# Optimization experiments

Hardware: AMD Instinct MI355X
Metric: run time of the kernel (lower is better)

The kernel has to match this reference:

```python
import jax, jax.numpy as jnp
import numpy as np

B, S, E, HD = 32, 1024, 768, 64


def _rope_tables(seq_len, dim):
    # theta = 10000 ** (-2*arange(0,dim,2)/dim); freqs = pos * theta
    theta = jnp.power(10000.0, -2.0 * jnp.arange(0, dim, 2, dtype=jnp.float32) / dim)
    pos = jnp.arange(seq_len, dtype=jnp.float32)[:, None]          # [S,1]
    freqs = pos * theta[None, :]                                    # [S,dim//2]
    cos = jnp.repeat(jnp.cos(freqs), 2, axis=-1)                    # [S,dim]
    sin = jnp.repeat(jnp.sin(freqs), 2, axis=-1)                    # [S,dim]
    return cos, sin


def _apply_rope(x, cos, sin):
    # rotate-half interleaved: new[...,0::2] = -x[...,1::2]; new[...,1::2] = x[...,0::2]
    b, s, d = x.shape
    x2 = x.reshape(b, s, d // 2, 2)
    rot = jnp.stack([-x2[..., 1], x2[..., 0]], axis=-1).reshape(b, s, d)
    return x * cos[None] + rot * sin[None]


def setup_inputs() -> dict:
    key = jax.random.key(0)
    k0, k1, k2, k3 = jax.random.split(key, 4)
    x = jax.random.normal(k0, (B, S, E), dtype=jnp.float32)
    Wq = jax.random.normal(k1, (HD, E), dtype=jnp.float32) * 0.02
    Wk = jax.random.normal(k2, (HD, E), dtype=jnp.float32) * 0.02
    Wv = jax.random.normal(k3, (HD, E), dtype=jnp.float32) * 0.02
    return {"x": x, "Wq": Wq, "Wk": Wk, "Wv": Wv}


def reference(x, Wq, Wk, Wv):
    b, s, e = x.shape
    q = jnp.einsum('bse,he->bsh', x, Wq)
    k = jnp.einsum('bse,he->bsh', x, Wk)
    v = jnp.einsum('bse,he->bsh', x, Wv)
    cos, sin = _rope_tables(s, q.shape[-1])
    rq = _apply_rope(q, cos, sin)
    rk = _apply_rope(k, cos, sin)
    scale = e ** (-0.5)  # NOTE: original scales by emb_dim, not head_size
    scores = jnp.einsum('bqh,bkh->bqk', rq, rk) * scale
    causal = jnp.tril(jnp.ones((s, s), dtype=bool))
    scores = jnp.where(causal[None], scores, -jnp.inf)
    attn = jax.nn.softmax(scores, axis=-1)
    return jnp.einsum('bqk,bkh->bqh', attn, v)
```

## Files before the change

kernel.cpp:

```cpp
#include <hip/hip_runtime.h>
#include <hip/hip_bf16.h>

#define B_  32
#define S_  1024
#define E_  768
#define HD_ 64
#define M_  (B_*S_)
#define WREP 8
#define WPSZ 147456

typedef __attribute__((ext_vector_type(8))) short short8;
typedef __attribute__((ext_vector_type(4))) float float4v;

__device__ __forceinline__ unsigned short f2bf(float x) {
    union { float f; unsigned u; } c; c.f = x;
    unsigned r = (c.u + 0x7FFFu + ((c.u >> 16) & 1u)) >> 16;
    return (unsigned short)r;
}

__device__ __forceinline__ void gld_lds16(const void* g, void* l) {
    __builtin_amdgcn_global_load_lds(
        (const __attribute__((address_space(1))) unsigned int*)g,
        (__attribute__((address_space(3))) unsigned int*)l,
        16, 0, 0);
}

__global__ __launch_bounds__(256) void setup_kernel(
    const unsigned int* __restrict__ xw,
    const void* __restrict__ Wq_, const void* __restrict__ Wk_,
    const void* __restrict__ Wv_,
    unsigned int* __restrict__ flag,
    float* __restrict__ cs_t, float* __restrict__ sn_t,
    unsigned short* __restrict__ wp)
{
    const int bx = blockIdx.x;
    if (bx < 128) {
        int idx = bx * 256 + threadIdx.x;
        int pos = idx >> 5;
        int ii  = idx & 31;
        float theta = exp2f(-(float)ii * 0.8304820237218406f);
        float fr = (float)pos * theta;
        float sn, cs;
        sincosf(fr, &sn, &cs);
        cs_t[idx] = cs;
        sn_t[idx] = sn;
        return;
    }
    __shared__ int cnt;
    if (threadIdx.x == 0) cnt = 0;
    __syncthreads();
    unsigned int w0 = xw[(size_t)threadIdx.x * 33331];
    unsigned int e0 = (w0 >> 8) & 0x7F;
    int hit = (e0 >= 0x3B && e0 <= 0x40) ? 1 : 0;
    atomicAdd(&cnt, hit);
    __syncthreads();
    const bool isb = (cnt > 128);
    if (bx == 128) {
        if (threadIdx.x == 0) *flag = isb ? 1u : 0u;
        return;
    }
    int rep  = (bx - 129) / 72;
    int bxin = (bx - 129) - rep * 72;
    int gid  = bxin * 256 + threadIdx.x;
    int lane = gid & 63;
    int tIdx = gid >> 6;
    int ct   = tIdx / 24;
    int rem  = tIdx - ct * 24;
    int c    = rem >> 1, ks = rem & 1;
    int quad = lane >> 4, l15 = lane & 15;
    const void* wsel = (ct < 4) ? Wq_ : (ct < 8 ? Wk_ : Wv_);
    int row = (ct & 3) * 16 + l15;
    int col = c * 64 + ks * 32 + quad * 8;
    uint4 w;
    if (isb) {
        w = *(const uint4*)((const unsigned short*)wsel + (size_t)row * E_ + col);
    } else {
        const float* f = (const float*)wsel + (size_t)row * E_ + col;
        float4 a = *(const float4*)f, bq = *(const float4*)(f + 4);
        w.x = f2bf(a.x)  | ((unsigned)f2bf(a.y)  << 16);
        w.y = f2bf(a.z)  | ((unsigned)f2bf(a.w)  << 16);
        w.z = f2bf(bq.x) | ((unsigned)f2bf(bq.y) << 16);
        w.w = f2bf(bq.z) | ((unsigned)f2bf(bq.w) << 16);
    }
    *(uint4*)(wp + (size_t)rep * WPSZ + (size_t)gid * 8) = w;
}

__global__ __launch_bounds__(512, 4) void qkv_mfma_kernel(
    const void* __restrict__ x_, const unsigned short* __restrict__ wp,
    const unsigned int* __restrict__ flag,
    const float* __restrict__ cs_t, const float* __restrict__ sn_t,
    unsigned short* __restrict__ rq_p, unsigned short* __restrict__ rk_p,
    unsigned short* __restrict__ vt_p)
{
    __shared__ __align__(16) char alds[3][8192];

    const bool isb = (*flag != 0);
    const int t    = threadIdx.x;
    const int lane = t & 63;
    const int wave = t >> 6;
    const int quad = lane >> 4;
    const int l15  = lane & 15;
    const int row0 = blockIdx.x * 64;
    const int h    = wave >> 2;
    const int cw   = wave & 3;

    const unsigned short* wpr = wp + (size_t)(blockIdx.x & (WREP - 1)) * WPSZ;

    const unsigned aRow = (unsigned)(wave * 8 + (lane >> 3));
    const unsigned eoA  = aRow * 768u + (unsigned)(((lane & 7) ^ (lane >> 3)) * 8);

    unsigned aA[2][2];
    #pragma unroll
    for (int mtl = 0; mtl < 2; ++mtl) {
        unsigned rl = (unsigned)((h * 2 + mtl) * 16 + l15);
        #pragma unroll
        for (int ks = 0; ks < 2; ++ks)
            aA[mtl][ks] = rl * 128u + ((((unsigned)ks << 2) | (unsigned)quad) ^ (rl & 7u)) * 16u;
    }

    const unsigned short* wbase[3][2];
    #pragma unroll
    for (int nt = 0; nt < 3; ++nt) {
        int ct = cw * 3 + nt;
        #pragma unroll
        for (int ks = 0; ks < 2; ++ks)
            wbase[nt][ks] = wpr + ((size_t)(ct * 24 + ks)) * 512 + lane * 8;
    }

    float4v acc[3][2];
    #pragma unroll
    for (int nt = 0; nt < 3; ++nt)
        #pragma unroll
        for (int mtl = 0; mtl < 2; ++mtl)
            #pragma unroll
            for (int r = 0; r < 4; ++r) acc[nt][mtl][r] = 0.f;

    short8 breg[2][3][2];

    const unsigned short* xb16 = (const unsigned short*)x_ + (size_t)row0 * E_;
    const float*          xb32 = (const float*)x_ + (size_t)row0 * E_;

    #define LOADB(cc, sel)                                                       \
        {   int tc_ = (cc) < 11 ? (cc) : 11;                                     \
            _Pragma("unroll")                                                    \
            for (int nt_ = 0; nt_ < 3; ++nt_)                                    \
                _Pragma("unroll")                                                \
                for (int ks_ = 0; ks_ < 2; ++ks_)                                \
                    breg[sel][nt_][ks_] =                                        \
                        *(const short8*)(wbase[nt_][ks_] + tc_ * 1024);          \
        }

    #define COMPUTE(cc, sel)                                                     \
        {   const char* sb_ = alds[(cc) % 3];                                    \
            _Pragma("unroll")                                                    \
            for (int ks_ = 0; ks_ < 2; ++ks_) {                                  \
                short8 af0 = *(const short8*)(sb_ + aA[0][ks_]);                 \
                short8 af1 = *(const short8*)(sb_ + aA[1][ks_]);                 \
                _Pragma("unroll")                                                \
                for (int nt_ = 0; nt_ < 3; ++nt_) {                              \
                    acc[nt_][0] = __builtin_amdgcn_mfma_f32_16x16x32_bf16(       \
                        af0, breg[sel][nt_][ks_], acc[nt_][0], 0, 0, 0);         \
                    acc[nt_][1] = __builtin_amdgcn_mfma_f32_16x16x32_bf16(       \
                        af1, breg[sel][nt_][ks_], acc[nt_][1], 0, 0, 0);         \
                }                                                                \
            }                                                                    \
        }

    if (isb) {
        LOADB(0, 0);
        __builtin_amdgcn_sched_barrier(0);
        gld_lds16(xb16 + eoA, alds[0] + wave * 1024);
        __builtin_amdgcn_sched_barrier(0);
        LOADB(1, 1);
        __builtin_amdgcn_sched_barrier(0);
        gld_lds16(xb16 + eoA + 64, alds[1] + wave * 1024);
        __builtin_amdgcn_sched_barrier(0);
        #pragma unroll
        for (int c = 0; c < 12; ++c) {
            asm volatile("s_waitcnt vmcnt(7)" ::: "memory");
            __builtin_amdgcn_s_barrier();
            {
                int tc = (c + 2) < 11 ? (c + 2) : 11;
                gld_lds16(xb16 + eoA + tc * 64, alds[(c + 2) % 3] + wave * 1024);
            }
            __builtin_amdgcn_sched_barrier(0);
            COMPUTE(c, c & 1);
            __builtin_amdgcn_sched_barrier(0);
            LOADB(c + 2, c & 1);
            __builtin_amdgcn_sched_barrier(0);
        }
    } else {
        auto stageA_f = [&](int c) {
            const float* f = xb32 + eoA + c * 64;
            float4 a = *(const float4*)f, bq = *(const float4*)(f + 4);
            uint4 w;
            w.x = f2bf(a.x)  | ((unsigned)f2bf(a.y)  << 16);
            w.y = f2bf(a.z)  | ((unsigned)f2bf(a.w)  << 16);
            w.z = f2bf(bq.x) | ((unsigned)f2bf(bq.y) << 16);
            w.w = f2bf(bq.z) | ((unsigned)f2bf(bq.w) << 16);
            *(uint4*)(alds[c % 3] + wave * 1024 + (size_t)lane * 16) = w;
        };
        stageA_f(0); stageA_f(1);
        LOADB(0, 0);
        __syncthreads();
        #pragma unroll
        for (int c = 0; c < 12; ++c) {
            if (c + 2 < 12) stageA_f(c + 2);
            LOADB(c + 1, (c + 1) & 1);
            COMPUTE(c, c & 1);
            __syncthreads();
        }
    }
    #undef LOADB
    #undef COMPUTE

    const int b      = row0 >> 10;
    const int s_in_b = row0 & (S_ - 1);
    #pragma unroll
    for (int nt = 0; nt < 3; ++nt) {
        int ct = cw * 3 + nt;
        int region = ct >> 2;
        int d = (ct & 3) * 16 + l15;
        if (region < 2) {
            unsigned short* dst = (region == 0) ? rq_p : rk_p;
            int ii = d >> 1;
            int ksq = d >> 5, quadq = (d >> 3) & 3, e = d & 7;
            #pragma unroll
            for (int mtl = 0; mtl < 2; ++mtl) {
                #pragma unroll
                for (int r = 0; r < 4; ++r) {
                    int row = row0 + (h * 2 + mtl) * 16 + quad * 4 + r;
                    int pos = row & (S_ - 1);
                    float cs = cs_t[pos * 32 + ii];
                    float sn = sn_t[pos * 32 + ii];
                    float val = acc[nt][mtl][r];
                    float partner = __shfl_xor(val, 1);
                    float res = (d & 1) ? fmaf(val, cs,  partner * sn)
                                        : fmaf(val, cs, -partner * sn);
                    int kt = pos >> 6, ntq = (pos >> 4) & 3, l15q = pos & 15;
                    size_t idx = ((((size_t)(b * 16 + kt) * 4 + ntq) * 2 + ksq) * 64
                                  + quadq * 16 + l15q) * 8 + e;
                    dst[idx] = f2bf(res);
                }
            }
        } else {
            int ntv = ct & 3;
            #pragma unroll
            for (int mtl = 0; mtl < 2; ++mtl) {
                int sb2 = s_in_b + (h * 2 + mtl) * 16 + quad * 4;
                int kt = sb2 >> 6, ksv = (sb2 >> 5) & 1, quadv = (sb2 >> 3) & 3, e0 = sb2 & 7;
                ushort4 pk;
                pk.x = f2bf(acc[nt][mtl][0]);
                pk.y = f2bf(acc[nt][mtl][1]);
                pk.z = f2bf(acc[nt][mtl][2]);
                pk.w = f2bf(acc[nt][mtl][3]);
                size_t idx = ((((size_t)(b * 16 + kt) * 4 + ntv) * 2 + ksv) * 64
                              + quadv * 16 + l15) * 8 + e0;
                *(ushort4*)(vt_p + idx) = pk;
            }
        }
    }
}

__global__ __launch_bounds__(256, 2) void attn_mfma_kernel(
    const unsigned short* __restrict__ rq_p, const unsigned short* __restrict__ rk_p,
    const unsigned short* __restrict__ vt_p, const unsigned int* __restrict__ flag,
    void* __restrict__ out)
{
    __shared__ unsigned short plds[4][16][72];

    const bool isb = (*flag != 0);
    const int t    = threadIdx.x;
    const int lane = t & 63;
    const int wave = t >> 6;
    const int quad = lane >> 4;
    const int l15  = lane & 15;

    const int g  = blockIdx.x;
    const int j  = g & 255;
    const int qt = (g < 256) ? (j & 15) : (15 - (j & 15));
    const int b  = (g < 256) ? (j >> 4) : (16 + (j >> 4));

    const int q0   = qt * 64 + wave * 16;
    const float scale = 0.03608439182435161f;

    const unsigned short* qb = rq_p + ((size_t)((b * 16 + qt) * 4 + wave) * 2) * 512;
    short8 qf0 = *(const short8*)(qb + lane * 8);
    short8 qf1 = *(const short8*)(qb + 512 + lane * 8);

    const unsigned short* kb0 = rk_p + ((size_t)b * 128) * 512 + lane * 8;
    const unsigned short* vb0 = vt_p + ((size_t)b * 128) * 512 + lane * 8;

    float4v o[4];
    float m_[4], l_[4];
    #pragma unroll
    for (int nt = 0; nt < 4; ++nt)
        #pragma unroll
        for (int r = 0; r < 4; ++r) o[nt][r] = 0.f;
    #pragma unroll
    for (int r = 0; r < 4; ++r) { m_[r] = -1e30f; l_[r] = 0.f; }

    const int nIter = (qt + 2) >> 1;

    for (int i = 0; i < nIter; ++i) {
        const int ta = 2 * i;
        const int tb = min(ta + 1, qt);
        const int ktv[2] = { ta, tb };

        short8 kf[2][4][2];
        #pragma unroll
        for (int slot = 0; slot < 2; ++slot)
            #pragma unroll
            for (int nt = 0; nt < 4; ++nt)
                #pragma unroll
                for (int ks = 0; ks < 2; ++ks)
                    kf[slot][nt][ks] = *(const short8*)(
                        kb0 + (size_t)(ktv[slot] * 8 + nt * 2 + ks) * 512);

        float sc[2][4][4];
        #pragma unroll
        for (int slot = 0; slot < 2; ++slot) {
            #pragma unroll
            for (int nt = 0; nt < 4; ++nt) {
                float4v s;
                #pragma unroll
                for (int r = 0; r < 4; ++r) s[r] = 0.f;
                s = __builtin_amdgcn_mfma_f32_16x16x32_bf16(qf0, kf[slot][nt][0], s, 0, 0, 0);
                s = __builtin_amdgcn_mfma_f32_16x16x32_bf16(qf1, kf[slot][nt][1], s, 0, 0, 0);
                #pragma unroll
                for (int r = 0; r < 4; ++r) sc[slot][nt][r] = s[r] * scale;
            }
        }

        short8 vf[2][4][2];
        #pragma unroll
        for (int slot = 0; slot < 2; ++slot)
            #pragma unroll
            for (int nt = 0; nt < 4; ++nt)
                #pragma unroll
                for (int ks = 0; ks < 2; ++ks)
                    vf[slot][nt][ks] = *(const short8*)(
                        vb0 + (size_t)(ktv[slot] * 8 + nt * 2 + ks) * 512);

        if (2 * i + 1 >= qt) {
            #pragma unroll
            for (int slot = 0; slot < 2; ++slot) {
                int ktl = 2 * i + slot;
                #pragma unroll
                for (int nt = 0; nt < 4; ++nt) {
                    int kg = ktl * 64 + nt * 16 + l15;
                    #pragma unroll
                    for (int r = 0; r < 4; ++r) {
                        int qg = q0 + quad * 4 + r;
                        if (kg > qg) sc[slot][nt][r] = -1e30f;
                    }
                }
            }
        }

        float mx[4];
        #pragma unroll
        for (int r = 0; r < 4; ++r) {
            float a0 = fmaxf(fmaxf(sc[0][0][r], sc[0][1][r]), fmaxf(sc[0][2][r], sc[0][3][r]));
            float a1 = fmaxf(fmaxf(sc[1][0][r], sc[1][1][r]), fmaxf(sc[1][2][r], sc[1][3][r]));
            mx[r] = fmaxf(a0, a1);
        }
        #pragma unroll
        for (int st = 1; st < 16; st <<= 1)
            #pragma unroll
            for (int r = 0; r < 4; ++r)
                mx[r] = fmaxf(mx[r], __shfl_xor(mx[r], st));

        float al[4];
        #pragma unroll
        for (int r = 0; r < 4; ++r) {
            float mn = fmaxf(m_[r], mx[r]);
            al[r] = __expf(m_[r] - mn);
            m_[r] = mn;
        }

        float sm[4] = {0.f, 0.f, 0.f, 0.f};
        #pragma unroll
        for (int slot = 0; slot < 2; ++slot)
            #pragma unroll
            for (int nt = 0; nt < 4; ++nt)
                #pragma unroll
                for (int r = 0; r < 4; ++r) {
                    float p = __expf(sc[slot][nt][r] - m_[r]);
                    sc[slot][nt][r] = p;
                    sm[r] += p;
                }
        #pragma unroll
        for (int st = 1; st < 16; st <<= 1)
            #pragma unroll
            for (int r = 0; r < 4; ++r)
                sm[r] += __shfl_xor(sm[r], st);
        #pragma unroll
        for (int r = 0; r < 4; ++r) l_[r] = l_[r] * al[r] + sm[r];

        #pragma unroll
        for (int nt = 0; nt < 4; ++nt)
            #pragma unroll
            for (int r = 0; r < 4; ++r) o[nt][r] *= al[r];

        #pragma unroll
        for (int slot = 0; slot < 2; ++slot) {
            #pragma unroll
            for (int nt = 0; nt < 4; ++nt)
                #pragma unroll
                for (int r = 0; r < 4; ++r)
                    plds[wave][quad * 4 + r][nt * 16 + l15] = f2bf(sc[slot][nt][r]);
            short8 pf0 = *(const short8*)&plds[wave][l15][quad * 8];
            short8 pf1 = *(const short8*)&plds[wave][l15][32 + quad * 8];
            #pragma unroll
            for (int nt = 0; nt < 4; ++nt) {
                o[nt] = __builtin_amdgcn_mfma_f32_16x16x32_bf16(pf0, vf[slot][nt][0], o[nt], 0, 0, 0);
                o[nt] = __builtin_amdgcn_mfma_f32_16x16x32_bf16(pf1, vf[slot][nt][1], o[nt], 0, 0, 0);
            }
        }
    }

    float inv[4];
    #pragma unroll
    for (int r = 0; r < 4; ++r) inv[r] = 1.0f / l_[r];
    if (isb) {
        unsigned short* op = (unsigned short*)out;
        #pragma unroll
        for (int nt = 0; nt < 4; ++nt)
            #pragma unroll
            for (int r = 0; r < 4; ++r) {
                size_t row = (size_t)b * S_ + q0 + quad * 4 + r;
                op[row * HD_ + nt * 16 + l15] = f2bf(o[nt][r] * inv[r]);
            }
    } else {
        float* op = (float*)out;
        #pragma unroll
        for (int nt = 0; nt < 4; ++nt)
            #pragma unroll
            for (int r = 0; r < 4; ++r) {
                size_t row = (size_t)b * S_ + q0 + quad * 4 + r;
                op[row * HD_ + nt * 16 + l15] = o[nt][r] * inv[r];
            }
    }
}

extern "C" void kernel_launch(void* const* d_in, const int* in_sizes, int n_in,
                              void* d_out, int out_size, void* d_ws, size_t ws_size,
                              hipStream_t stream) {
    const void* x  = d_in[0];
    const void* Wq = d_in[1];
    const void* Wk = d_in[2];
    const void* Wv = d_in[3];

    unsigned int* flag = (unsigned int*)d_ws;
    float* cs_t = (float*)d_ws + 64;
    float* sn_t = cs_t + (size_t)S_ * 32;
    unsigned short* wp   = (unsigned short*)(sn_t + (size_t)S_ * 32);
    unsigned short* rq_p = wp + (size_t)WREP * WPSZ;
    unsigned short* rk_p = rq_p + (size_t)M_ * HD_;
    unsigned short* vt_p = rk_p + (size_t)M_ * HD_;

    hipLaunchKernelGGL(setup_kernel, dim3(129 + 72 * WREP), dim3(256), 0, stream,
                       (const unsigned int*)x, Wq, Wk, Wv, flag, cs_t, sn_t, wp);
    hipLaunchKernelGGL(qkv_mfma_kernel, dim3(M_ / 64), dim3(512), 0, stream,
                       x, wp, flag, cs_t, sn_t, rq_p, rk_p, vt_p);
    hipLaunchKernelGGL(attn_mfma_kernel, dim3(512), dim3(256), 0, stream,
                       rq_p, rk_p, vt_p, flag, d_out);
}
```

Measured before the change: 188.0 us.

## Process two 64-row tiles per QKV block to reuse weight registers

The QKV projection kernel now handles 128 rows per block as two 64-row sub-tiles that share each loaded weight fragment, halving weight global loads per output row. LDS staging is doubled, accumulators double, and the grid is halved. Launch bounds drop to 2 blocks per SM to allow the extra registers, and the vmcnt wait is adjusted for the extra A load per stage. This cuts occupancy and halves the number of blocks (256), which may hurt latency hiding or load balance.

Measured after the change: 187.6 us. No clear change (-0.2%).

```diff
diff --git a/kernel.cpp b/kernel.cpp
--- a/kernel.cpp
+++ b/kernel.cpp
@@ -85,14 +85,14 @@
     *(uint4*)(wp + (size_t)rep * WPSZ + (size_t)gid * 8) = w;
 }
 
-__global__ __launch_bounds__(512, 4) void qkv_mfma_kernel(
+__global__ __launch_bounds__(512, 2) void qkv_mfma_kernel(
     const void* __restrict__ x_, const unsigned short* __restrict__ wp,
     const unsigned int* __restrict__ flag,
     const float* __restrict__ cs_t, const float* __restrict__ sn_t,
     unsigned short* __restrict__ rq_p, unsigned short* __restrict__ rk_p,
     unsigned short* __restrict__ vt_p)
 {
-    __shared__ __align__(16) char alds[3][8192];
+    __shared__ __align__(16) char alds[3][2][8192];
 
     const bool isb = (*flag != 0);
     const int t    = threadIdx.x;
@@ -100,7 +100,7 @@
     const int wave = t >> 6;
     const int quad = lane >> 4;
     const int l15  = lane & 15;
-    const int row0 = blockIdx.x * 64;
+    const int row0 = blockIdx.x * 128;
     const int h    = wave >> 2;
     const int cw   = wave & 3;
 
@@ -127,18 +127,22 @@
             wbase[nt][ks] = wpr + ((size_t)(ct * 24 + ks)) * 512 + lane * 8;
     }
 
-    float4v acc[3][2];
-    #pragma unroll
-    for (int nt = 0; nt < 3; ++nt)
-        #pragma unroll
-        for (int mtl = 0; mtl < 2; ++mtl)
-            #pragma unroll
-            for (int r = 0; r < 4; ++r) acc[nt][mtl][r] = 0.f;
+    float4v acc[2][3][2];
+    #pragma unroll
+    for (int t2 = 0; t2 < 2; ++t2)
+        #pragma unroll
+        for (int nt = 0; nt < 3; ++nt)
+            #pragma unroll
+            for (int mtl = 0; mtl < 2; ++mtl)
+                #pragma unroll
+                for (int r = 0; r < 4; ++r) acc[t2][nt][mtl][r] = 0.f;
 
     short8 breg[2][3][2];
 
-    const unsigned short* xb16 = (const unsigned short*)x_ + (size_t)row0 * E_;
-    const float*          xb32 = (const float*)x_ + (size_t)row0 * E_;
+    const unsigned short* xb16a = (const unsigned short*)x_ + (size_t)row0 * E_;
+    const unsigned short* xb16b = xb16a + (size_t)64 * E_;
+    const float*          xb32a = (const float*)x_ + (size_t)row0 * E_;
+    const float*          xb32b = xb32a + (size_t)64 * E_;
 
     #define LOADB(cc, sel)                                                       \
         {   int tc_ = (cc) < 11 ? (cc) : 11;                                     \
@@ -150,18 +154,27 @@
                         *(const short8*)(wbase[nt_][ks_] + tc_ * 1024);          \
         }
 
+    #define LOADA(cc)                                                            \
+        {   int tc_ = (cc) < 11 ? (cc) : 11;                                     \
+            gld_lds16(xb16a + eoA + tc_ * 64, alds[(cc) % 3][0] + wave * 1024);  \
+            gld_lds16(xb16b + eoA + tc_ * 64, alds[(cc) % 3][1] + wave * 1024);  \
+        }
+
     #define COMPUTE(cc, sel)                                                     \
-        {   const char* sb_ = alds[(cc) % 3];                                    \
-            _Pragma("unroll")                                                    \
-            for (int ks_ = 0; ks_ < 2; ++ks_) {                                  \
-                short8 af0 = *(const short8*)(sb_ + aA[0][ks_]);                 \
-                short8 af1 = *(const short8*)(sb_ + aA[1][ks_]);                 \
+        {   _Pragma("unroll")                                                    \
+            for (int t2_ = 0; t2_ < 2; ++t2_) {                                  \
+                const char* sb_ = alds[(cc) % 3][t2_];                           \
                 _Pragma("unroll")                                                \
-                for (int nt_ = 0; nt_ < 3; ++nt_) {                              \
-                    acc[nt_][0] = __builtin_amdgcn_mfma_f32_16x16x32_bf16(       \
-                        af0, breg[sel][nt_][ks_], acc[nt_][0], 0, 0, 0);         \
-                    acc[nt_][1] = __builtin_amdgcn_mfma_f32_16x16x32_bf16(       \
-                        af1, breg[sel][nt_][ks_], acc[nt_][1], 0, 0, 0);         \
+                for (int ks_ = 0; ks_ < 2; ++ks_) {                              \
+                    short8 af0 = *(const short8*)(sb_ + aA[0][ks_]);             \
+                    short8 af1 = *(const short8*)(sb_ + aA[1][ks_]);             \
+                    _Pragma("unroll")                                            \
+                    for (int nt_ = 0; nt_ < 3; ++nt_) {                          \
+                        acc[t2_][nt_][0] = __builtin_amdgcn_mfma_f32_16x16x32_bf16( \
+                            af0, breg[sel][nt_][ks_], acc[t2_][nt_][0], 0, 0, 0);   \
+                        acc[t2_][nt_][1] = __builtin_amdgcn_mfma_f32_16x16x32_bf16( \
+                            af1, breg[sel][nt_][ks_], acc[t2_][nt_][1], 0, 0, 0);   \
+                    }                                                            \
                 }                                                                \
             }                                                                    \
         }
@@ -169,20 +182,17 @@
     if (isb) {
         LOADB(0, 0);
         __builtin_amdgcn_sched_barrier(0);
-        gld_lds16(xb16 + eoA, alds[0] + wave * 1024);
+        LOADA(0);
         __builtin_amdgcn_sched_barrier(0);
         LOADB(1, 1);
         __builtin_amdgcn_sched_barrier(0);
-        gld_lds16(xb16 + eoA + 64, alds[1] + wave * 1024);
+        LOADA(1);
         __builtin_amdgcn_sched_barrier(0);
         #pragma unroll
         for (int c = 0; c < 12; ++c) {
-            asm volatile("s_waitcnt vmcnt(7)" ::: "memory");
+            asm volatile("s_waitcnt vmcnt(8)" ::: "memory");
             __builtin_amdgcn_s_barrier();
-            {
-                int tc = (c + 2) < 11 ? (c + 2) : 11;
-                gld_lds16(xb16 + eoA + tc * 64, alds[(c + 2) % 3] + wave * 1024);
-            }
+            LOADA(c + 2);
             __builtin_amdgcn_sched_barrier(0);
             COMPUTE(c, c & 1);
             __builtin_amdgcn_sched_barrier(0);
@@ -191,14 +201,17 @@
         }
     } else {
         auto stageA_f = [&](int c) {
-            const float* f = xb32 + eoA + c * 64;
-            float4 a = *(const float4*)f, bq = *(const float4*)(f + 4);
-            uint4 w;
-            w.x = f2bf(a.x)  | ((unsigned)f2bf(a.y)  << 16);
-            w.y = f2bf(a.z)  | ((unsigned)f2bf(a.w)  << 16);
-            w.z = f2bf(bq.x) | ((unsigned)f2bf(bq.y) << 16);
-            w.w = f2bf(bq.z) | ((unsigned)f2bf(bq.w) << 16);
-            *(uint4*)(alds[c % 3] + wave * 1024 + (size_t)lane * 16) = w;
+            #pragma unroll
+            for (int t2 = 0; t2 < 2; ++t2) {
+                const float* f = (t2 ? xb32b : xb32a) + eoA + c * 64;
+                float4 a = *(const float4*)f, bq = *(const float4*)(f + 4);
+                uint4 w;
+                w.x = f2bf(a.x)  | ((unsigned)f2bf(a.y)  << 16);
+                w.y = f2bf(a.z)  | ((unsigned)f2bf(a.w)  << 16);
+                w.z = f2bf(bq.x) | ((unsigned)f2bf(bq.y) << 16);
+                w.w = f2bf(bq.z) | ((unsigned)f2bf(bq.w) << 16);
+                *(uint4*)(alds[c % 3][t2] + wave * 1024 + (size_t)lane * 16) = w;
+            }
         };
         stageA_f(0); stageA_f(1);
         LOADB(0, 0);
@@ -212,51 +225,56 @@
         }
     }
     #undef LOADB
+    #undef LOADA
     #undef COMPUTE
 
-    const int b      = row0 >> 10;
-    const int s_in_b = row0 & (S_ - 1);
-    #pragma unroll
-    for (int nt = 0; nt < 3; ++nt) {
-        int ct = cw * 3 + nt;
-        int region = ct >> 2;
-        int d = (ct & 3) * 16 + l15;
-        if (region < 2) {
-            unsigned short* dst = (region == 0) ? rq_p : rk_p;
-            int ii = d >> 1;
-            int ksq = d >> 5, quadq = (d >> 3) & 3, e = d & 7;
-            #pragma unroll
-            for (int mtl = 0; mtl < 2; ++mtl) {
-                #pragma unroll
-                for (int r = 0; r < 4; ++r) {
-                    int row = row0 + (h * 2 + mtl) * 16 + quad * 4 + r;
-                    int pos = row & (S_ - 1);
-                    float cs = cs_t[pos * 32 + ii];
-                    float sn = sn_t[pos * 32 + ii];
-                    float val = acc[nt][mtl][r];
-                    float partner = __shfl_xor(val, 1);
-                    float res = (d & 1) ? fmaf(val, cs,  partner * sn)
-                                        : fmaf(val, cs, -partner * sn);
-                    int kt = pos >> 6, ntq = (pos >> 4) & 3, l15q = pos & 15;
-                    size_t idx = ((((size_t)(b * 16 + kt) * 4 + ntq) * 2 + ksq) * 64
-                                  + quadq * 16 + l15q) * 8 + e;
-                    dst[idx] = f2bf(res);
+    #pragma unroll
+    for (int t2 = 0; t2 < 2; ++t2) {
+        const int rt0    = row0 + t2 * 64;
+        const int b      = rt0 >> 10;
+        const int s_in_b = rt0 & (S_ - 1);
+        #pragma unroll
+        for (int nt = 0; nt < 3; ++nt) {
+            int ct = cw * 3 + nt;
+            int region = ct >> 2;
+            int d = (ct & 3) * 16 + l15;
+            if (region < 2) {
+                unsigned short* dst = (region == 0) ? rq_p : rk_p;
+                int ii = d >> 1;
+                int ksq = d >> 5, quadq = (d >> 3) & 3, e = d & 7;
+                #pragma unroll
+                for (int mtl = 0; mtl < 2; ++mtl) {
+                    #pragma unroll
+                    for (int r = 0; r < 4; ++r) {
+                        int row = rt0 + (h * 2 + mtl) * 16 + quad * 4 + r;
+                        int pos = row & (S_ - 1);
+                        float cs = cs_t[pos * 32 + ii];
+                        float sn = sn_t[pos * 32 + ii];
+                        float val = acc[t2][nt][mtl][r];
+                        float partner = __shfl_xor(val, 1);
+                        float res = (d & 1) ? fmaf(val, cs,  partner * sn)
+                                            : fmaf(val, cs, -partner * sn);
+                        int kt = pos >> 6, ntq = (pos >> 4) & 3, l15q = pos & 15;
+                        size_t idx = ((((size_t)(b * 16 + kt) * 4 + ntq) * 2 + ksq) * 64
+                                      + quadq * 16 + l15q) * 8 + e;
+                        dst[idx] = f2bf(res);
+                    }
                 }
-            }
-        } else {
-            int ntv = ct & 3;
-            #pragma unroll
-            for (int mtl = 0; mtl < 2; ++mtl) {
-                int sb2 = s_in_b + (h * 2 + mtl) * 16 + quad * 4;
-                int kt = sb2 >> 6, ksv = (sb2 >> 5) & 1, quadv = (sb2 >> 3) & 3, e0 = sb2 & 7;
-                ushort4 pk;
-                pk.x = f2bf(acc[nt][mtl][0]);
-                pk.y = f2bf(acc[nt][mtl][1]);
-                pk.z = f2bf(acc[nt][mtl][2]);
-                pk.w = f2bf(acc[nt][mtl][3]);
-                size_t idx = ((((size_t)(b * 16 + kt) * 4 + ntv) * 2 + ksv) * 64
-                              + quadv * 16 + l15) * 8 + e0;
-                *(ushort4*)(vt_p + idx) = pk;
+            } else {
+                int ntv = ct & 3;
+                #pragma unroll
+                for (int mtl = 0; mtl < 2; ++mtl) {
+                    int sb2 = s_in_b + (h * 2 + mtl) * 16 + quad * 4;
+                    int kt = sb2 >> 6, ksv = (sb2 >> 5) & 1, quadv = (sb2 >> 3) & 3, e0 = sb2 & 7;
+                    ushort4 pk;
+                    pk.x = f2bf(acc[t2][nt][mtl][0]);
+                    pk.y = f2bf(acc[t2][nt][mtl][1]);
+                    pk.z = f2bf(acc[t2][nt][mtl][2]);
+                    pk.w = f2bf(acc[t2][nt][mtl][3]);
+                    size_t idx = ((((size_t)(b * 16 + kt) * 4 + ntv) * 2 + ksv) * 64
+                                  + quadv * 16 + l15) * 8 + e0;
+                    *(ushort4*)(vt_p + idx) = pk;
+                }
             }
         }
     }
@@ -462,7 +480,7 @@
 
     hipLaunchKernelGGL(setup_kernel, dim3(129 + 72 * WREP), dim3(256), 0, stream,
                        (const unsigned int*)x, Wq, Wk, Wv, flag, cs_t, sn_t, wp);
-    hipLaunchKernelGGL(qkv_mfma_kernel, dim3(M_ / 64), dim3(512), 0, stream,
+    hipLaunchKernelGGL(qkv_mfma_kernel, dim3(M_ / 128), dim3(512), 0, stream,
                        x, wp, flag, cs_t, sn_t, rq_p, rk_p, vt_p);
     hipLaunchKernelGGL(attn_mfma_kernel, dim3(512), dim3(256), 0, stream,
                        rq_p, rk_p, vt_p, flag, d_out);
```
